# Optimization experiments

Hardware: AMD Instinct MI355X
Metric: run time of the kernel (lower is better)

The kernel has to match this reference:

```python
import jax, jax.numpy as jnp
import numpy as np

B, L, D = 4, 2048, 1024

def setup_inputs() -> dict:
    key = jax.random.key(0)
    k = jax.random.split(key, 5)
    s = 1.0 / np.sqrt(D)
    return {
        "x": jax.random.normal(k[0], (B, L, D), dtype=jnp.float32),
        "W1": jax.random.uniform(k[1], (D, D), jnp.float32, -s, s),
        "b1": jax.random.uniform(k[2], (D,), jnp.float32, -s, s),
        "W2": jax.random.uniform(k[3], (D, D), jnp.float32, -s, s),
        "b2": jax.random.uniform(k[4], (D,), jnp.float32, -s, s),
    }

def reference(x, W1, b1, W2, b2):
    # query = fc1(x), value = fc2(x); torch Linear: x @ W^T + b
    query = jnp.einsum("bld,ed->ble", x, W1) + b1   # [B,L,D]
    value = jnp.einsum("bld,ed->ble", x, W2) + b2   # [B,L,D]
    # attn = softmax(query @ value^T)  (dot attention, no scaling in original)
    scores = jnp.einsum("bqd,bkd->bqk", query, value)  # [B,L,L]
    attn = jax.nn.softmax(scores, axis=-1)
    # dropout_p=0.0 -> identity
    return jnp.einsum("bqk,bkd->bqd", attn, value)     # [B,L,D]
```

## Files before the change

kernel.cpp:

```cpp
#include <hip/hip_runtime.h>
#include <stdint.h>
#include <stddef.h>


typedef _Float16  f16_t;
typedef _Float16  f16x8  __attribute__((ext_vector_type(8)));
typedef float     f32x4  __attribute__((ext_vector_type(4)));

__device__ __forceinline__ f32x4 mfma16(f16x8 a, f16x8 b, f32x4 c) {
  return __builtin_amdgcn_mfma_f32_16x16x32_f16(a, b, c, 0, 0, 0);
}

__device__ __forceinline__ void async_copy16(const f16_t* g, f16_t* l) {
  __builtin_amdgcn_global_load_lds(
      (const __attribute__((address_space(1))) unsigned int*)(g),
      (__attribute__((address_space(3))) unsigned int*)(l),
      16, 0, 0);
}

__device__ __forceinline__ void gemm_core(
    const f16_t* __restrict__ A, const f16_t* __restrict__ B,
    int lda, int ldb, int nk,
    f16_t* As, f16_t* Bs, f32x4 acc[4][4])
{
  const int tid  = threadIdx.x;
  const int lane = tid & 63;
  const int w    = tid >> 6;
  const int wr   = (w >> 1) * 64;
  const int wc   = (w & 1) * 64;
  const int quad = lane >> 4;
  const int l16  = lane & 15;

  const int r0  = tid >> 2;
  const int kc0 = (tid & 3) * 8;

  const f16_t* Ag0 = A + (size_t)r0 * lda + kc0;
  const f16_t* Ag1 = A + (size_t)(r0 + 64) * lda + kc0;
  const f16_t* Bg0 = B + (size_t)r0 * ldb + kc0;
  const f16_t* Bg1 = B + (size_t)(r0 + 64) * ldb + kc0;
  f16_t* Al0 = As + tid * 8;
  f16_t* Al1 = As + (tid + 256) * 8;
  f16_t* Bl0 = Bs + tid * 8;
  f16_t* Bl1 = Bs + (tid + 256) * 8;

  for (int kt = 0; kt < nk; ++kt) {
    async_copy16(Ag0, Al0);
    async_copy16(Ag1, Al1);
    async_copy16(Bg0, Bl0);
    async_copy16(Bg1, Bl1);
    __syncthreads();

    f16x8 af[4], bfr[4];
#pragma unroll
    for (int i = 0; i < 4; ++i) {
      af[i]  = *(const f16x8*)(As + (wr + i * 16 + l16) * 32 + quad * 8);
      bfr[i] = *(const f16x8*)(Bs + (wc + i * 16 + l16) * 32 + quad * 8);
    }
#pragma unroll
    for (int i = 0; i < 4; ++i)
#pragma unroll
      for (int j = 0; j < 4; ++j)
        acc[i][j] = mfma16(af[i], bfr[j], acc[i][j]);

    __syncthreads();
    Ag0 += 32; Ag1 += 32; Bg0 += 32; Bg1 += 32;
  }
}

__global__ __launch_bounds__(256) void cvt_kernel(
    const float* __restrict__ in, f16_t* __restrict__ out)
{
  const size_t i = ((size_t)blockIdx.x * 256 + threadIdx.x) * 8;
  f32x4 a = *(const f32x4*)(in + i);
  f32x4 b = *(const f32x4*)(in + i + 4);
  f16x8 o;
#pragma unroll
  for (int k = 0; k < 4; ++k) { o[k] = (f16_t)a[k]; o[k + 4] = (f16_t)b[k]; }
  *(f16x8*)(out + i) = o;
}

__global__ __launch_bounds__(256) void proj_kernel(
    const f16_t* __restrict__ X, const f16_t* __restrict__ W,
    const float* __restrict__ bias, f16_t* __restrict__ Out,
    f16_t* __restrict__ OutT)
{
  __shared__ __align__(16) f16_t As[128 * 32];
  __shared__ __align__(16) f16_t Bs[128 * 32];
  const int m0 = blockIdx.x * 128;
  const int n0 = blockIdx.y * 128;

  f32x4 acc[4][4] = {};
  gemm_core(X + (size_t)m0 * 1024, W + (size_t)n0 * 1024,
            1024, 1024, 1024 / 32, As, Bs, acc);

  const int lane = threadIdx.x & 63;
  const int w    = threadIdx.x >> 6;
  const int wr   = (w >> 1) * 64, wc = (w & 1) * 64;
  const int quad = lane >> 4,     l16 = lane & 15;

#pragma unroll
  for (int j = 0; j < 4; ++j) {
    const int col = n0 + wc + j * 16 + l16;
    const float bj = bias[col];
#pragma unroll
    for (int i = 0; i < 4; ++i) {
#pragma unroll
      for (int r = 0; r < 4; ++r) {
        const int row = m0 + wr + i * 16 + quad * 4 + r;
        const float v = acc[i][j][r] + bj;
        Out[(size_t)row * 1024 + col] = (f16_t)v;
        if (OutT) {
          const int b = row >> 11, key = row & 2047;
          OutT[(((size_t)b << 10) + col) * 2048 + key] = (f16_t)v;
        }
      }
    }
  }
}

__global__ __launch_bounds__(256) void score_kernel(
    const f16_t* __restrict__ Q, const f16_t* __restrict__ V,
    float* __restrict__ S)
{
  __shared__ __align__(16) f16_t As[128 * 32];
  __shared__ __align__(16) f16_t Bs[128 * 32];
  const int m0 = blockIdx.x * 128;
  const int n0 = blockIdx.y * 128;
  const size_t boff = (size_t)blockIdx.z * 2048 * 1024;

  f32x4 acc[4][4] = {};
  gemm_core(Q + boff + (size_t)m0 * 1024, V + boff + (size_t)n0 * 1024,
            1024, 1024, 1024 / 32, As, Bs, acc);

  float* Sb = S + (size_t)blockIdx.z * 2048 * 2048;
  const int lane = threadIdx.x & 63;
  const int w    = threadIdx.x >> 6;
  const int wr   = (w >> 1) * 64, wc = (w & 1) * 64;
  const int quad = lane >> 4,     l16 = lane & 15;

#pragma unroll
  for (int i = 0; i < 4; ++i)
#pragma unroll
    for (int j = 0; j < 4; ++j)
#pragma unroll
      for (int r = 0; r < 4; ++r) {
        const int row = m0 + wr + i * 16 + quad * 4 + r;
        const int col = n0 + wc + j * 16 + l16;
        Sb[(size_t)row * 2048 + col] = acc[i][j][r];
      }
}

__global__ __launch_bounds__(256) void softmax_kernel(float* __restrict__ S)
{
  float* src = S + (size_t)blockIdx.x * 2048;
  f16_t* dst = (f16_t*)src;
  const int tid  = threadIdx.x;
  const int lane = tid & 63;
  const int w    = tid >> 6;

  f32x4 va = *((const f32x4*)src + tid * 2);
  f32x4 vb = *((const f32x4*)src + tid * 2 + 1);
  float f[8];
#pragma unroll
  for (int k = 0; k < 4; ++k) { f[k] = va[k]; f[k + 4] = vb[k]; }

  float m = f[0];
#pragma unroll
  for (int k = 1; k < 8; ++k) m = fmaxf(m, f[k]);
#pragma unroll
  for (int off = 32; off >= 1; off >>= 1) m = fmaxf(m, __shfl_xor(m, off));

  __shared__ float red[4];
  if (lane == 0) red[w] = m;
  __syncthreads();
  m = fmaxf(fmaxf(red[0], red[1]), fmaxf(red[2], red[3]));

  float s = 0.f;
#pragma unroll
  for (int k = 0; k < 8; ++k) { f[k] = __expf(f[k] - m); s += f[k]; }
#pragma unroll
  for (int off = 32; off >= 1; off >>= 1) s += __shfl_xor(s, off);
  __syncthreads();
  if (lane == 0) red[w] = s;
  __syncthreads();
  s = (red[0] + red[1]) + (red[2] + red[3]);
  const float inv = 1.f / s;

  f16x8 o;
#pragma unroll
  for (int k = 0; k < 8; ++k) o[k] = (f16_t)(f[k] * inv);
  *((f16x8*)dst + tid) = o;
}

__global__ __launch_bounds__(256) void out_kernel(
    const f16_t* __restrict__ P, const f16_t* __restrict__ Vt,
    float* __restrict__ Out)
{
  __shared__ __align__(16) f16_t As[128 * 32];
  __shared__ __align__(16) f16_t Bs[128 * 32];
  const int m0 = blockIdx.x * 128;
  const int n0 = blockIdx.y * 128;
  const size_t poff  = (size_t)blockIdx.z * 2048 * 4096;
  const size_t vtoff = (size_t)blockIdx.z * 1024 * 2048;

  f32x4 acc[4][4] = {};
  gemm_core(P + poff + (size_t)m0 * 4096, Vt + vtoff + (size_t)n0 * 2048,
            4096, 2048, 2048 / 32, As, Bs, acc);

  float* Ob = Out + (size_t)blockIdx.z * 2048 * 1024;
  const int lane = threadIdx.x & 63;
  const int w    = threadIdx.x >> 6;
  const int wr   = (w >> 1) * 64, wc = (w & 1) * 64;
  const int quad = lane >> 4,     l16 = lane & 15;

#pragma unroll
  for (int i = 0; i < 4; ++i)
#pragma unroll
    for (int j = 0; j < 4; ++j)
#pragma unroll
      for (int r = 0; r < 4; ++r) {
        const int row = m0 + wr + i * 16 + quad * 4 + r;
        const int col = n0 + wc + j * 16 + l16;
        Ob[(size_t)row * 1024 + col] = acc[i][j][r];
      }
}

extern "C" void kernel_launch(void* const* d_in, const int* in_sizes, int n_in,
                              void* d_out, int out_size, void* d_ws, size_t ws_size,
                              hipStream_t stream) {
  const float* x  = (const float*)d_in[0];
  const float* W1 = (const float*)d_in[1];
  const float* b1 = (const float*)d_in[2];
  const float* W2 = (const float*)d_in[3];
  const float* b2 = (const float*)d_in[4];
  float* out = (float*)d_out;

  const size_t QN = (size_t)8192 * 1024;
  const size_t WN = (size_t)1024 * 1024;
  f16_t* xh  = (f16_t*)d_ws;
  f16_t* W1h = xh + QN;
  f16_t* W2h = W1h + WN;
  f16_t* Q   = W2h + WN;
  f16_t* V   = Q + QN;
  f16_t* Vt  = V + QN;
  float* S   = (float*)(Vt + QN);

  dim3 blk(256);
  cvt_kernel<<<4096, blk, 0, stream>>>(x, xh);
  cvt_kernel<<<512, blk, 0, stream>>>(W1, W1h);
  cvt_kernel<<<512, blk, 0, stream>>>(W2, W2h);
  proj_kernel<<<dim3(64, 8), blk, 0, stream>>>(xh, W1h, b1, Q, nullptr);
  proj_kernel<<<dim3(64, 8), blk, 0, stream>>>(xh, W2h, b2, V, Vt);
  score_kernel<<<dim3(16, 16, 4), blk, 0, stream>>>(Q, V, S);
  softmax_kernel<<<8192, blk, 0, stream>>>(S);
  out_kernel<<<dim3(16, 8, 4), blk, 0, stream>>>((const f16_t*)S, Vt, out);
}
```

Measured before the change: 276.7 us.

## Fuse Q/V projections, swizzle LDS tiles, stage Vt transpose, enlarge score tiles

Merges the two projection GEMMs into one kernel that loads each X tile once and accumulates both Q and V. The transposed V is now staged through LDS and written as coalesced 16-byte stores instead of scattered 2-byte stores. The LDS layout gains an XOR swizzle to reduce bank conflicts on fragment reads, and the score GEMM moves to 256x128 tiles. In exchange, register and LDS use per block go up, which may lower occupancy.

```diff
diff --git a/kernel.cpp b/kernel.cpp
--- a/kernel.cpp
+++ b/kernel.cpp
@@ -4,8 +4,9 @@
 
 
 typedef _Float16  f16_t;
-typedef _Float16  f16x8  __attribute__((ext_vector_type(8)));
-typedef float     f32x4  __attribute__((ext_vector_type(4)));
+typedef _Float16  f16x8 __attribute__((ext_vector_type(8)));
+typedef _Float16  f16x4 __attribute__((ext_vector_type(4)));
+typedef float     f32x4 __attribute__((ext_vector_type(4)));
 
 __device__ __forceinline__ f32x4 mfma16(f16x8 a, f16x8 b, f32x4 c) {
   return __builtin_amdgcn_mfma_f32_16x16x32_f16(a, b, c, 0, 0, 0);
@@ -18,11 +19,79 @@
       16, 0, 0);
 }
 
+template <int RT>
 __device__ __forceinline__ void gemm_core(
     const f16_t* __restrict__ A, const f16_t* __restrict__ B,
     int lda, int ldb, int nk,
-    f16_t* As, f16_t* Bs, f32x4 acc[4][4])
-{
+    f16_t* __restrict__ As, f16_t* __restrict__ Bs, f32x4 (&acc)[RT][4])
+{
+  const int tid  = threadIdx.x;
+  const int lane = tid & 63;
+  const int w    = tid >> 6;
+  const int wr   = (w >> 1) * (RT * 16);
+  const int wc   = (w & 1) * 64;
+  const int quad = lane >> 4;
+  const int l16  = lane & 15;
+  const int sw   = (quad ^ ((l16 >> 1) & 3)) * 8;
+
+  const int r0  = tid >> 2;
+  const int kc0 = ((tid & 3) ^ ((r0 >> 1) & 3)) * 8;
+
+  const f16_t* Ag = A + (size_t)r0 * lda + kc0;
+  const f16_t* Bg = B + (size_t)r0 * ldb + kc0;
+
+  for (int kt = 0; kt < nk; ++kt) {
+#pragma unroll
+    for (int h = 0; h < RT / 2; ++h)
+      async_copy16(Ag + (size_t)(64 * h) * lda, As + (tid + 256 * h) * 8);
+    async_copy16(Bg, Bs + tid * 8);
+    async_copy16(Bg + (size_t)64 * ldb, Bs + (tid + 256) * 8);
+    __syncthreads();
+
+    f16x8 af[RT], bf[4];
+#pragma unroll
+    for (int i = 0; i < RT; ++i)
+      af[i] = *(const f16x8*)(As + (wr + i * 16 + l16) * 32 + sw);
+#pragma unroll
+    for (int j = 0; j < 4; ++j)
+      bf[j] = *(const f16x8*)(Bs + (wc + j * 16 + l16) * 32 + sw);
+#pragma unroll
+    for (int i = 0; i < RT; ++i)
+#pragma unroll
+      for (int j = 0; j < 4; ++j)
+        acc[i][j] = mfma16(af[i], bf[j], acc[i][j]);
+
+    __syncthreads();
+    Ag += 32; Bg += 32;
+  }
+}
+
+__global__ __launch_bounds__(256) void cvt_kernel(
+    const float* __restrict__ in, f16_t* __restrict__ out)
+{
+  const size_t i = ((size_t)blockIdx.x * 256 + threadIdx.x) * 8;
+  f32x4 a = *(const f32x4*)(in + i);
+  f32x4 b = *(const f32x4*)(in + i + 4);
+  f16x8 o;
+#pragma unroll
+  for (int k = 0; k < 4; ++k) { o[k] = (f16_t)a[k]; o[k + 4] = (f16_t)b[k]; }
+  *(f16x8*)(out + i) = o;
+}
+
+__global__ __launch_bounds__(256) void proj_qv_kernel(
+    const f16_t* __restrict__ X, const f16_t* __restrict__ W1,
+    const f16_t* __restrict__ W2, const float* __restrict__ b1,
+    const float* __restrict__ b2, f16_t* __restrict__ Q,
+    f16_t* __restrict__ V, f16_t* __restrict__ Vt)
+{
+  __shared__ __align__(16) f16_t Xs[128 * 32];
+  __shared__ __align__(16) f16_t W1s[128 * 32];
+  __shared__ __align__(16) f16_t W2s[128 * 32];
+  __shared__ __align__(16) f16_t Ts[128 * 136];
+
+  const int m0 = blockIdx.x * 128;
+  const int n0 = blockIdx.y * 128;
+
   const int tid  = threadIdx.x;
   const int lane = tid & 63;
   const int w    = tid >> 6;
@@ -30,91 +99,74 @@
   const int wc   = (w & 1) * 64;
   const int quad = lane >> 4;
   const int l16  = lane & 15;
-
-  const int r0  = tid >> 2;
-  const int kc0 = (tid & 3) * 8;
-
-  const f16_t* Ag0 = A + (size_t)r0 * lda + kc0;
-  const f16_t* Ag1 = A + (size_t)(r0 + 64) * lda + kc0;
-  const f16_t* Bg0 = B + (size_t)r0 * ldb + kc0;
-  const f16_t* Bg1 = B + (size_t)(r0 + 64) * ldb + kc0;
-  f16_t* Al0 = As + tid * 8;
-  f16_t* Al1 = As + (tid + 256) * 8;
-  f16_t* Bl0 = Bs + tid * 8;
-  f16_t* Bl1 = Bs + (tid + 256) * 8;
-
-  for (int kt = 0; kt < nk; ++kt) {
-    async_copy16(Ag0, Al0);
-    async_copy16(Ag1, Al1);
-    async_copy16(Bg0, Bl0);
-    async_copy16(Bg1, Bl1);
+  const int sw   = (quad ^ ((l16 >> 1) & 3)) * 8;
+  const int r0   = tid >> 2;
+  const int kc0  = ((tid & 3) ^ ((r0 >> 1) & 3)) * 8;
+
+  const f16_t* Xg = X + (size_t)(m0 + r0) * 1024 + kc0;
+  const f16_t* G1 = W1 + (size_t)(n0 + r0) * 1024 + kc0;
+  const f16_t* G2 = W2 + (size_t)(n0 + r0) * 1024 + kc0;
+
+  f32x4 accQ[4][4] = {};
+  f32x4 accV[4][4] = {};
+
+  for (int kt = 0; kt < 32; ++kt) {
+    async_copy16(Xg,                      Xs + tid * 8);
+    async_copy16(Xg + (size_t)64 * 1024,  Xs + (tid + 256) * 8);
+    async_copy16(G1,                      W1s + tid * 8);
+    async_copy16(G1 + (size_t)64 * 1024,  W1s + (tid + 256) * 8);
+    async_copy16(G2,                      W2s + tid * 8);
+    async_copy16(G2 + (size_t)64 * 1024,  W2s + (tid + 256) * 8);
     __syncthreads();
 
-    f16x8 af[4], bfr[4];
+    f16x8 xf[4], w1f[4], w2f[4];
 #pragma unroll
     for (int i = 0; i < 4; ++i) {
-      af[i]  = *(const f16x8*)(As + (wr + i * 16 + l16) * 32 + quad * 8);
-      bfr[i] = *(const f16x8*)(Bs + (wc + i * 16 + l16) * 32 + quad * 8);
+      xf[i]  = *(const f16x8*)(Xs  + (wr + i * 16 + l16) * 32 + sw);
+      w1f[i] = *(const f16x8*)(W1s + (wc + i * 16 + l16) * 32 + sw);
+      w2f[i] = *(const f16x8*)(W2s + (wc + i * 16 + l16) * 32 + sw);
     }
 #pragma unroll
     for (int i = 0; i < 4; ++i)
 #pragma unroll
-      for (int j = 0; j < 4; ++j)
-        acc[i][j] = mfma16(af[i], bfr[j], acc[i][j]);
-
+      for (int j = 0; j < 4; ++j) {
+        accQ[i][j] = mfma16(xf[i], w1f[j], accQ[i][j]);
+        accV[i][j] = mfma16(xf[i], w2f[j], accV[i][j]);
+      }
     __syncthreads();
-    Ag0 += 32; Ag1 += 32; Bg0 += 32; Bg1 += 32;
+    Xg += 32; G1 += 32; G2 += 32;
   }
-}
-
-__global__ __launch_bounds__(256) void cvt_kernel(
-    const float* __restrict__ in, f16_t* __restrict__ out)
-{
-  const size_t i = ((size_t)blockIdx.x * 256 + threadIdx.x) * 8;
-  f32x4 a = *(const f32x4*)(in + i);
-  f32x4 b = *(const f32x4*)(in + i + 4);
-  f16x8 o;
-#pragma unroll
-  for (int k = 0; k < 4; ++k) { o[k] = (f16_t)a[k]; o[k + 4] = (f16_t)b[k]; }
-  *(f16x8*)(out + i) = o;
-}
-
-__global__ __launch_bounds__(256) void proj_kernel(
-    const f16_t* __restrict__ X, const f16_t* __restrict__ W,
-    const float* __restrict__ bias, f16_t* __restrict__ Out,
-    f16_t* __restrict__ OutT)
-{
-  __shared__ __align__(16) f16_t As[128 * 32];
-  __shared__ __align__(16) f16_t Bs[128 * 32];
-  const int m0 = blockIdx.x * 128;
-  const int n0 = blockIdx.y * 128;
-
-  f32x4 acc[4][4] = {};
-  gemm_core(X + (size_t)m0 * 1024, W + (size_t)n0 * 1024,
-            1024, 1024, 1024 / 32, As, Bs, acc);
-
-  const int lane = threadIdx.x & 63;
-  const int w    = threadIdx.x >> 6;
-  const int wr   = (w >> 1) * 64, wc = (w & 1) * 64;
-  const int quad = lane >> 4,     l16 = lane & 15;
 
 #pragma unroll
   for (int j = 0; j < 4; ++j) {
-    const int col = n0 + wc + j * 16 + l16;
-    const float bj = bias[col];
+    const int cl  = wc + j * 16 + l16;
+    const int col = n0 + cl;
+    const float bq = b1[col], bv = b2[col];
 #pragma unroll
     for (int i = 0; i < 4; ++i) {
+      const int rowb = wr + i * 16 + quad * 4;
+      f16x4 tv;
 #pragma unroll
       for (int r = 0; r < 4; ++r) {
-        const int row = m0 + wr + i * 16 + quad * 4 + r;
-        const float v = acc[i][j][r] + bj;
-        Out[(size_t)row * 1024 + col] = (f16_t)v;
-        if (OutT) {
-          const int b = row >> 11, key = row & 2047;
-          OutT[(((size_t)b << 10) + col) * 2048 + key] = (f16_t)v;
-        }
+        const int row = m0 + rowb + r;
+        const float q = accQ[i][j][r] + bq;
+        const float v = accV[i][j][r] + bv;
+        Q[(size_t)row * 1024 + col] = (f16_t)q;
+        V[(size_t)row * 1024 + col] = (f16_t)v;
+        tv[r] = (f16_t)v;
       }
+      *(f16x4*)(&Ts[cl * 136 + rowb]) = tv;
     }
+  }
+  __syncthreads();
+
+  const size_t vtbase = ((size_t)(m0 >> 11) << 21) + (size_t)n0 * 2048 + (m0 & 2047);
+#pragma unroll
+  for (int rep = 0; rep < 8; ++rep) {
+    const int idx = rep * 256 + tid;
+    const int c = idx >> 4, ch = idx & 15;
+    f16x8 vv = *(const f16x8*)(&Ts[c * 136 + ch * 8]);
+    *(f16x8*)(&Vt[vtbase + (size_t)c * 2048 + ch * 8]) = vv;
   }
 }
 
@@ -122,24 +174,24 @@
     const f16_t* __restrict__ Q, const f16_t* __restrict__ V,
     float* __restrict__ S)
 {
-  __shared__ __align__(16) f16_t As[128 * 32];
+  __shared__ __align__(16) f16_t As[256 * 32];
   __shared__ __align__(16) f16_t Bs[128 * 32];
-  const int m0 = blockIdx.x * 128;
+  const int m0 = blockIdx.x * 256;
   const int n0 = blockIdx.y * 128;
   const size_t boff = (size_t)blockIdx.z * 2048 * 1024;
 
-  f32x4 acc[4][4] = {};
-  gemm_core(Q + boff + (size_t)m0 * 1024, V + boff + (size_t)n0 * 1024,
-            1024, 1024, 1024 / 32, As, Bs, acc);
+  f32x4 acc[8][4] = {};
+  gemm_core<8>(Q + boff + (size_t)m0 * 1024, V + boff + (size_t)n0 * 1024,
+               1024, 1024, 1024 / 32, As, Bs, acc);
 
   float* Sb = S + (size_t)blockIdx.z * 2048 * 2048;
   const int lane = threadIdx.x & 63;
   const int w    = threadIdx.x >> 6;
-  const int wr   = (w >> 1) * 64, wc = (w & 1) * 64;
-  const int quad = lane >> 4,     l16 = lane & 15;
-
-#pragma unroll
-  for (int i = 0; i < 4; ++i)
+  const int wr   = (w >> 1) * 128, wc = (w & 1) * 64;
+  const int quad = lane >> 4,      l16 = lane & 15;
+
+#pragma unroll
+  for (int i = 0; i < 8; ++i)
 #pragma unroll
     for (int j = 0; j < 4; ++j)
 #pragma unroll
@@ -204,8 +256,8 @@
   const size_t vtoff = (size_t)blockIdx.z * 1024 * 2048;
 
   f32x4 acc[4][4] = {};
-  gemm_core(P + poff + (size_t)m0 * 4096, Vt + vtoff + (size_t)n0 * 2048,
-            4096, 2048, 2048 / 32, As, Bs, acc);
+  gemm_core<4>(P + poff + (size_t)m0 * 4096, Vt + vtoff + (size_t)n0 * 2048,
+               4096, 2048, 2048 / 32, As, Bs, acc);
 
   float* Ob = Out + (size_t)blockIdx.z * 2048 * 1024;
   const int lane = threadIdx.x & 63;
@@ -249,9 +301,8 @@
   cvt_kernel<<<4096, blk, 0, stream>>>(x, xh);
   cvt_kernel<<<512, blk, 0, stream>>>(W1, W1h);
   cvt_kernel<<<512, blk, 0, stream>>>(W2, W2h);
-  proj_kernel<<<dim3(64, 8), blk, 0, stream>>>(xh, W1h, b1, Q, nullptr);
-  proj_kernel<<<dim3(64, 8), blk, 0, stream>>>(xh, W2h, b2, V, Vt);
-  score_kernel<<<dim3(16, 16, 4), blk, 0, stream>>>(Q, V, S);
+  proj_qv_kernel<<<dim3(64, 8), blk, 0, stream>>>(xh, W1h, W2h, b1, b2, Q, V, Vt);
+  score_kernel<<<dim3(8, 16, 4), blk, 0, stream>>>(Q, V, S);
   softmax_kernel<<<8192, blk, 0, stream>>>(S);
   out_kernel<<<dim3(16, 8, 4), blk, 0, stream>>>((const f16_t*)S, Vt, out);
 }
```

Result: slower. 311.7 us (+12.6%).
